# Optimization experiments

Hardware: AMD Instinct MI355X
Metric: run time of the kernel (lower is better)

## Reference

```python
import jax, jax.numpy as jnp
import numpy as np


def _gcn_conv(x, W, b, src, dst, dinv):
    # h = x @ W, then symmetric-normalized aggregation with self-loops (PyG GCNConv)
    n = x.shape[0]
    h = x @ W  # [N, H]
    norm_e = dinv[src] * dinv[dst]  # [E]
    msgs = h[src] * norm_e[:, None]  # [E, H] gathered+scaled messages
    agg = jax.ops.segment_sum(msgs, dst, num_segments=n)
    # self-loop contribution: norm = dinv[i]^2
    agg = agg + h * (dinv * dinv)[:, None]
    return agg + b


def setup_inputs() -> dict:
    key = jax.random.key(0)
    k1, k2, k3, k4, k5 = jax.random.split(key, 5)
    N, E, C_in, H = 50000, 800000, 256, 128
    x = jax.random.normal(k1, (N, C_in), dtype=jnp.float32)
    edge_index = jax.random.randint(k2, (2, E), 0, N, dtype=jnp.int32)
    s = 1.0 / np.sqrt(C_in)
    W1 = jax.random.uniform(k3, (C_in, H), jnp.float32, -s, s)
    b1 = jnp.zeros((H,), jnp.float32)
    s2 = 1.0 / np.sqrt(H)
    W_mu = jax.random.uniform(k4, (H, H), jnp.float32, -s2, s2)
    b_mu = jnp.zeros((H,), jnp.float32)
    W_ls = jax.random.uniform(k5, (H, H), jnp.float32, -s2, s2)
    b_ls = jnp.zeros((H,), jnp.float32)
    return {"x": x, "edge_index": edge_index, "W1": W1, "b1": b1,
            "W_mu": W_mu, "b_mu": b_mu, "W_ls": W_ls, "b_ls": b_ls}


def reference(x, edge_index, W1, b1, W_mu, b_mu, W_ls, b_ls):
    n = x.shape[0]
    src, dst = edge_index[0], edge_index[1]
    # degree with self-loops (count incoming edges at target + 1)
    deg = jax.ops.segment_sum(jnp.ones_like(dst, dtype=x.dtype), dst, num_segments=n) + 1.0
    dinv = jax.lax.rsqrt(deg)
    h = jax.nn.relu(_gcn_conv(x, W1, b1, src, dst, dinv))
    mu = _gcn_conv(h, W_mu, b_mu, src, dst, dinv)
    logstd = _gcn_conv(h, W_ls, b_ls, src, dst, dinv)
    return mu, logstd
```

## Files before the change

### kernel.cpp

```cpp
#include <hip/hip_runtime.h>
#include <hip/hip_bf16.h>
#include <cstdint>

#define HFEAT 128
#define CIN   256

typedef unsigned int  uint;
typedef unsigned short ushort;
typedef short bf16x8 __attribute__((ext_vector_type(8)));
typedef float f32x4  __attribute__((ext_vector_type(4)));

__device__ inline float bflo(uint u){ return __uint_as_float(u << 16); }
__device__ inline float bfhi(uint u){ return __uint_as_float(u & 0xffff0000u); }
__device__ inline uint  f2bf(float f){
  union { __hip_bfloat16 b; ushort u; } cvt;
  cvt.b = __float2bfloat16(f);
  return (uint)cvt.u;
}


__global__ void k_count(const int* __restrict__ dst, int E, int* __restrict__ counts){
  int e = blockIdx.x*blockDim.x + threadIdx.x;
  if (e < E) atomicAdd(&counts[dst[e]], 1);
}

__global__ void k_scan1(const int* __restrict__ counts, int n,
                        int* __restrict__ excl, int* __restrict__ bsum,
                        float* __restrict__ dinv){
  __shared__ int sm[1024];
  int t = threadIdx.x;
  int i = blockIdx.x*1024 + t;
  int v = (i < n) ? counts[i] : 0;
  if (i < n) dinv[i] = rsqrtf((float)v + 1.0f);
  sm[t] = v;
  __syncthreads();
  for (int off = 1; off < 1024; off <<= 1){
    int add = (t >= off) ? sm[t-off] : 0;
    __syncthreads();
    sm[t] += add;
    __syncthreads();
  }
  if (i < n) excl[i] = sm[t] - v;
  if (t == 1023) bsum[blockIdx.x] = sm[t];
}

__global__ void k_scan2(int* __restrict__ bsum, int nb){
  if (threadIdx.x == 0 && blockIdx.x == 0){
    int run = 0;
    for (int b = 0; b < nb; b++){ int v = bsum[b]; bsum[b] = run; run += v; }
  }
}

__global__ void k_scan3(const int* __restrict__ bsum, int n, int E,
                        int* __restrict__ rowoff, int* __restrict__ cursor){
  int i = blockIdx.x*blockDim.x + threadIdx.x;
  if (i < n){
    int v = rowoff[i] + bsum[blockIdx.x];
    rowoff[i] = v;
    cursor[i] = v;
  }
  if (i == 0) rowoff[n] = E;
}

__global__ void k_fill(const int* __restrict__ src, const int* __restrict__ dst, int E,
                       int* __restrict__ cursor, int* __restrict__ csr4){
  int e = blockIdx.x*blockDim.x + threadIdx.x;
  if (e < E){
    int pos = atomicAdd(&cursor[dst[e]], 1);
    csr4[pos] = src[e];
  }
}


__global__ void k_cvt_all(const float* __restrict__ W1,  const float* __restrict__ Wmu,
                          const float* __restrict__ Wls, ushort* __restrict__ W1t,
                          ushort* __restrict__ Wmut, ushort* __restrict__ Wlst){
  int b = blockIdx.x, t = threadIdx.x;
  if (b < 128){
    W1t[b * CIN + t] = (ushort)f2bf(W1[(size_t)t * HFEAT + b]);
  } else if (b < 256){
    int nn = b - 128;
    if (t < HFEAT) Wmut[nn * HFEAT + t] = (ushort)f2bf(Wmu[(size_t)t * HFEAT + nn]);
  } else {
    int nn = b - 256;
    if (t < HFEAT) Wlst[nn * HFEAT + t] = (ushort)f2bf(Wls[(size_t)t * HFEAT + nn]);
  }
}


template<int K, bool IN_BF16, bool BIAS, bool OUT_BF16, bool SCALE_DINV>
__global__ void __launch_bounds__(256) k_gemm_mfma(const void* __restrict__ Ain,
                                                   const ushort* __restrict__ Wta,
                                                   const ushort* __restrict__ Wtb,
                                                   const float* __restrict__ ba,
                                                   const float* __restrict__ bb,
                                                   const float* __restrict__ dinv,
                                                   void* __restrict__ outa,
                                                   void* __restrict__ outb,
                                                   int n){
  __shared__ ushort Abuf[64][72];
  __shared__ ushort Bbuf[128][72];

  const ushort* Wt   = (blockIdx.y == 0) ? Wta : Wtb;
  const float*  bias = (blockIdx.y == 0) ? ba  : bb;
  void*         outv = (blockIdx.y == 0) ? outa : outb;

  const int tid  = threadIdx.x;
  const int w    = tid >> 6;
  const int l    = tid & 63;
  const int l15  = l & 15;
  const int lhi  = l >> 4;
  const int row0 = blockIdx.x * 64;

  const int ar = tid >> 2;
  const int aq = tid & 3;
  int arow = row0 + ar; if (arow >= n) arow = n - 1;

  f32x4 acc[8];
  #pragma unroll
  for (int t = 0; t < 8; t++) acc[t] = (f32x4){0.f, 0.f, 0.f, 0.f};

  const int NT = K / 64;
  #pragma unroll
  for (int kt = 0; kt < NT; ++kt){
    if (IN_BF16){
      const ushort* ap = (const ushort*)Ain + (size_t)arow * K + aq * 16 + kt * 64;
      uint4 v0 = *(const uint4*)(ap);
      uint4 v1 = *(const uint4*)(ap + 8);
      *(uint4*)&Abuf[ar][aq * 16]     = v0;
      *(uint4*)&Abuf[ar][aq * 16 + 8] = v1;
    } else {
      const float* p = (const float*)Ain + (size_t)arow * K + aq * 16 + kt * 64;
      float4 v0 = *(const float4*)(p);
      float4 v1 = *(const float4*)(p + 4);
      float4 v2 = *(const float4*)(p + 8);
      float4 v3 = *(const float4*)(p + 12);
      uint4 pa, pb;
      pa.x = f2bf(v0.x) | (f2bf(v0.y) << 16);
      pa.y = f2bf(v0.z) | (f2bf(v0.w) << 16);
      pa.z = f2bf(v1.x) | (f2bf(v1.y) << 16);
      pa.w = f2bf(v1.z) | (f2bf(v1.w) << 16);
      pb.x = f2bf(v2.x) | (f2bf(v2.y) << 16);
      pb.y = f2bf(v2.z) | (f2bf(v2.w) << 16);
      pb.z = f2bf(v3.x) | (f2bf(v3.y) << 16);
      pb.w = f2bf(v3.z) | (f2bf(v3.w) << 16);
      *(uint4*)&Abuf[ar][aq * 16]     = pa;
      *(uint4*)&Abuf[ar][aq * 16 + 8] = pb;
    }
    #pragma unroll
    for (int j = 0; j < 4; ++j){
      int flat = tid + 256 * j;
      int bn = flat >> 3;
      int bk = (flat & 7) * 8;
      uint4 v = *(const uint4*)(Wt + (size_t)bn * K + kt * 64 + bk);
      *(uint4*)&Bbuf[bn][bk] = v;
    }
    __syncthreads();

    #pragma unroll
    for (int ks = 0; ks < 2; ++ks){
      const int ko = ks * 32 + lhi * 8;
      bf16x8 af = *(bf16x8*)&Abuf[16 * w + l15][ko];
      #pragma unroll
      for (int nt = 0; nt < 8; ++nt){
        bf16x8 bf = *(bf16x8*)&Bbuf[nt * 16 + l15][ko];
        acc[nt] = __builtin_amdgcn_mfma_f32_16x16x32_bf16(af, bf, acc[nt], 0, 0, 0);
      }
    }
    __syncthreads();
  }

  float bv[8];
  #pragma unroll
  for (int nt = 0; nt < 8; ++nt) bv[nt] = BIAS ? bias[nt * 16 + l15] : 0.f;

  #pragma unroll
  for (int j = 0; j < 4; ++j){
    int r = row0 + 16 * w + lhi * 4 + j;
    if (r < n){
      float sc = SCALE_DINV ? dinv[r] : 1.f;
      if (OUT_BF16){
        ushort* orow = (ushort*)outv + (size_t)r * HFEAT + l15;
        #pragma unroll
        for (int nt = 0; nt < 8; ++nt)
          orow[nt * 16] = (ushort)f2bf((acc[nt][j] + bv[nt]) * sc);
      } else {
        float* orow = (float*)outv + (size_t)r * HFEAT + l15;
        #pragma unroll
        for (int nt = 0; nt < 8; ++nt)
          orow[nt * 16] = acc[nt][j] + bv[nt];
      }
    }
  }
}


template<int RELU>
__global__ void __launch_bounds__(256) k_agg(const ushort* __restrict__ in,
                                             const float* __restrict__ bias,
                                             const int* __restrict__ rowoff,
                                             const int* __restrict__ csr4,
                                             const float* __restrict__ dinv,
                                             ushort* __restrict__ out, int n){
  int gid  = blockIdx.x*blockDim.x + threadIdx.x;
  int node = gid >> 6;
  int lane = gid & 63;
  if (node >= n) return;
  const int w  = lane >> 4;
  const int q  = lane & 15;
  const int f0 = q * 8;

  float acc[8] = {0,0,0,0,0,0,0,0};

  const int e0 = rowoff[node], e1 = rowoff[node+1];
  #pragma unroll 2
  for (int e = e0 + w; e < e1; e += 4){
    int s = csr4[e];
    uint4 v = *(const uint4*)(in + ((size_t)s << 7) + f0);
    acc[0] += bflo(v.x); acc[1] += bfhi(v.x);
    acc[2] += bflo(v.y); acc[3] += bfhi(v.y);
    acc[4] += bflo(v.z); acc[5] += bfhi(v.z);
    acc[6] += bflo(v.w); acc[7] += bfhi(v.w);
  }
  if (w == 0){
    uint4 v = *(const uint4*)(in + ((size_t)node << 7) + f0);
    acc[0] += bflo(v.x); acc[1] += bfhi(v.x);
    acc[2] += bflo(v.y); acc[3] += bfhi(v.y);
    acc[4] += bflo(v.z); acc[5] += bfhi(v.z);
    acc[6] += bflo(v.w); acc[7] += bfhi(v.w);
  }
  #pragma unroll
  for (int j = 0; j < 8; j++){
    acc[j] += __shfl_xor(acc[j], 16);
    acc[j] += __shfl_xor(acc[j], 32);
  }

  if (w == 0){
    float di = dinv[node];
    uint4 p;
    if (RELU){
      float4 b0 = *(const float4*)&bias[f0];
      float4 b1 = *(const float4*)&bias[f0 + 4];
      float r0 = fmaxf(fmaf(acc[0], di, b0.x), 0.f) * di;
      float r1 = fmaxf(fmaf(acc[1], di, b0.y), 0.f) * di;
      float r2 = fmaxf(fmaf(acc[2], di, b0.z), 0.f) * di;
      float r3 = fmaxf(fmaf(acc[3], di, b0.w), 0.f) * di;
      float r4 = fmaxf(fmaf(acc[4], di, b1.x), 0.f) * di;
      float r5 = fmaxf(fmaf(acc[5], di, b1.y), 0.f) * di;
      float r6 = fmaxf(fmaf(acc[6], di, b1.z), 0.f) * di;
      float r7 = fmaxf(fmaf(acc[7], di, b1.w), 0.f) * di;
      p.x = f2bf(r0) | (f2bf(r1) << 16);
      p.y = f2bf(r2) | (f2bf(r3) << 16);
      p.z = f2bf(r4) | (f2bf(r5) << 16);
      p.w = f2bf(r6) | (f2bf(r7) << 16);
    } else {
      p.x = f2bf(acc[0] * di) | (f2bf(acc[1] * di) << 16);
      p.y = f2bf(acc[2] * di) | (f2bf(acc[3] * di) << 16);
      p.z = f2bf(acc[4] * di) | (f2bf(acc[5] * di) << 16);
      p.w = f2bf(acc[6] * di) | (f2bf(acc[7] * di) << 16);
    }
    *(uint4*)(out + ((size_t)node << 7) + f0) = p;
  }
}


extern "C" void kernel_launch(void* const* d_in, const int* in_sizes, int n_in,
                              void* d_out, int out_size, void* d_ws, size_t ws_size,
                              hipStream_t stream){
  const float* x   = (const float*)d_in[0];
  const int*   ei  = (const int*)  d_in[1];
  const float* W1  = (const float*)d_in[2];
  const float* b1  = (const float*)d_in[3];
  const float* Wmu = (const float*)d_in[4];
  const float* bmu = (const float*)d_in[5];
  const float* Wls = (const float*)d_in[6];
  const float* bls = (const float*)d_in[7];
  int N = in_sizes[0] / CIN;
  int E = in_sizes[1] / 2;
  const int* src = ei;
  const int* dst = ei + E;
  float* out = (float*)d_out;

  char* w = (char*)d_ws;
  auto alloc = [&](size_t bytes)->char*{
    char* p = w; w += (bytes + 255) & ~(size_t)255; return p;
  };
  ushort* t1    = (ushort*)alloc((size_t)N*HFEAT*2);
  ushort* t2    = (ushort*)alloc((size_t)N*HFEAT*2);
  ushort* gb    = (ushort*)alloc((size_t)N*HFEAT*2);
  ushort* W1bt  = (ushort*)alloc((size_t)HFEAT*CIN*2);
  ushort* Wmut  = (ushort*)alloc((size_t)HFEAT*HFEAT*2);
  ushort* Wlst  = (ushort*)alloc((size_t)HFEAT*HFEAT*2);
  int*   counts = (int*)   alloc((size_t)N*4);
  float* dinv   = (float*) alloc((size_t)N*4);
  int*   rowoff = (int*)   alloc(((size_t)N+1)*4);
  int*   cursor = (int*)   alloc((size_t)N*4);
  int*   bsum   = (int*)   alloc(256*4);
  int*   csr4   = (int*)   alloc((size_t)E*4);

  int nbE  = (E + 255) / 256;
  int nbS  = (N + 1023) / 1024;
  int nbG  = (N + 63) / 64;

  hipMemsetAsync(counts, 0, (size_t)N*4, stream);
  k_count   <<<nbE, 256, 0, stream>>>(dst, E, counts);
  k_scan1   <<<nbS, 1024, 0, stream>>>(counts, N, rowoff, bsum, dinv);
  k_scan2   <<<1, 64, 0, stream>>>(bsum, nbS);
  k_scan3   <<<nbS, 1024, 0, stream>>>(bsum, N, E, rowoff, cursor);
  k_fill    <<<nbE, 256, 0, stream>>>(src, dst, E, cursor, csr4);
  k_cvt_all <<<384, 256, 0, stream>>>(W1, Wmu, Wls, W1bt, Wmut, Wlst);

  k_gemm_mfma<CIN, false, false, true, true><<<dim3(nbG, 1), 256, 0, stream>>>(
      x, W1bt, W1bt, nullptr, nullptr, dinv, t1, t1, N);
  int aggBlocks = (int)(((size_t)N*64 + 255) / 256);
  k_agg<1><<<aggBlocks, 256, 0, stream>>>(t1, b1, rowoff, csr4, dinv, t2, N);
  k_agg<0><<<aggBlocks, 256, 0, stream>>>(t2, nullptr, rowoff, csr4, dinv, gb, N);
  k_gemm_mfma<HFEAT, true, true, false, false><<<dim3(nbG, 2), 256, 0, stream>>>(
      gb, Wmut, Wlst, bmu, bls, nullptr, out, out + (size_t)N*HFEAT, N);
}
```

Measured before the change: 295.3 us.

## Fuse degree count with first GEMM and build CSR from atomic ranks

Edge degree counting now runs in the same launch as the first MFMA GEMM, and each atomic increment records the edge's rank. Because of that, the per-row dinv scaling moves out of the GEMM epilogue and into the aggregation as a per-edge dinv[src] weight. The CSR fill writes each edge to rowoff plus its rank with no second atomic pass. Source indices are stored as 16-bit values to halve index traffic, which only works while N stays below 65536. The serial block-sum scan becomes a shared-memory parallel scan, and the aggregation gains one extra dinv gather per edge.

```diff
diff --git a/kernel.cpp b/kernel.cpp
--- a/kernel.cpp
+++ b/kernel.cpp
@@ -18,11 +18,6 @@
   return (uint)cvt.u;
 }
 
-
-__global__ void k_count(const int* __restrict__ dst, int E, int* __restrict__ counts){
-  int e = blockIdx.x*blockDim.x + threadIdx.x;
-  if (e < E) atomicAdd(&counts[dst[e]], 1);
-}
 
 __global__ void k_scan1(const int* __restrict__ counts, int n,
                         int* __restrict__ excl, int* __restrict__ bsum,
@@ -45,30 +40,32 @@
 }
 
 __global__ void k_scan2(int* __restrict__ bsum, int nb){
-  if (threadIdx.x == 0 && blockIdx.x == 0){
-    int run = 0;
-    for (int b = 0; b < nb; b++){ int v = bsum[b]; bsum[b] = run; run += v; }
-  }
+  __shared__ int sm[1024];
+  int t = threadIdx.x;
+  int v = (t < nb) ? bsum[t] : 0;
+  sm[t] = v;
+  __syncthreads();
+  for (int off = 1; off < 1024; off <<= 1){
+    int add = (t >= off) ? sm[t-off] : 0;
+    __syncthreads();
+    sm[t] += add;
+    __syncthreads();
+  }
+  if (t < nb) bsum[t] = sm[t] - v;
 }
 
 __global__ void k_scan3(const int* __restrict__ bsum, int n, int E,
-                        int* __restrict__ rowoff, int* __restrict__ cursor){
+                        int* __restrict__ rowoff){
   int i = blockIdx.x*blockDim.x + threadIdx.x;
-  if (i < n){
-    int v = rowoff[i] + bsum[blockIdx.x];
-    rowoff[i] = v;
-    cursor[i] = v;
-  }
+  if (i < n) rowoff[i] += bsum[blockIdx.x];
   if (i == 0) rowoff[n] = E;
 }
 
-__global__ void k_fill(const int* __restrict__ src, const int* __restrict__ dst, int E,
-                       int* __restrict__ cursor, int* __restrict__ csr4){
+__global__ void k_fill(const int* __restrict__ src, const int* __restrict__ dst,
+                       const int* __restrict__ rank, int E,
+                       const int* __restrict__ rowoff, ushort* __restrict__ csr2){
   int e = blockIdx.x*blockDim.x + threadIdx.x;
-  if (e < E){
-    int pos = atomicAdd(&cursor[dst[e]], 1);
-    csr4[pos] = src[e];
-  }
+  if (e < E) csr2[rowoff[dst[e]] + rank[e]] = (ushort)src[e];
 }
 
 
@@ -88,29 +85,20 @@
 }
 
 
-template<int K, bool IN_BF16, bool BIAS, bool OUT_BF16, bool SCALE_DINV>
-__global__ void __launch_bounds__(256) k_gemm_mfma(const void* __restrict__ Ain,
-                                                   const ushort* __restrict__ Wta,
-                                                   const ushort* __restrict__ Wtb,
-                                                   const float* __restrict__ ba,
-                                                   const float* __restrict__ bb,
-                                                   const float* __restrict__ dinv,
-                                                   void* __restrict__ outa,
-                                                   void* __restrict__ outb,
-                                                   int n){
-  __shared__ ushort Abuf[64][72];
-  __shared__ ushort Bbuf[128][72];
-
-  const ushort* Wt   = (blockIdx.y == 0) ? Wta : Wtb;
-  const float*  bias = (blockIdx.y == 0) ? ba  : bb;
-  void*         outv = (blockIdx.y == 0) ? outa : outb;
-
+template<int K, bool IN_BF16, bool BIAS, bool OUT_BF16>
+__device__ __forceinline__ void gemm_body(int bid,
+                                          const void* __restrict__ Ain,
+                                          const ushort* __restrict__ Wt,
+                                          const float* __restrict__ bias,
+                                          void* __restrict__ outv,
+                                          int n,
+                                          ushort (*Abuf)[72], ushort (*Bbuf)[72]){
   const int tid  = threadIdx.x;
   const int w    = tid >> 6;
   const int l    = tid & 63;
   const int l15  = l & 15;
   const int lhi  = l >> 4;
-  const int row0 = blockIdx.x * 64;
+  const int row0 = bid * 64;
 
   const int ar = tid >> 2;
   const int aq = tid & 3;
@@ -178,12 +166,11 @@
   for (int j = 0; j < 4; ++j){
     int r = row0 + 16 * w + lhi * 4 + j;
     if (r < n){
-      float sc = SCALE_DINV ? dinv[r] : 1.f;
       if (OUT_BF16){
         ushort* orow = (ushort*)outv + (size_t)r * HFEAT + l15;
         #pragma unroll
         for (int nt = 0; nt < 8; ++nt)
-          orow[nt * 16] = (ushort)f2bf((acc[nt][j] + bv[nt]) * sc);
+          orow[nt * 16] = (ushort)f2bf(acc[nt][j] + bv[nt]);
       } else {
         float* orow = (float*)outv + (size_t)r * HFEAT + l15;
         #pragma unroll
@@ -195,11 +182,47 @@
 }
 
 
+__global__ void __launch_bounds__(256) k_count_gemm1(const int* __restrict__ dst, int E,
+                                                     int* __restrict__ counts,
+                                                     int* __restrict__ rank,
+                                                     int nbE,
+                                                     const float* __restrict__ x,
+                                                     const ushort* __restrict__ W1t,
+                                                     ushort* __restrict__ t1, int n){
+  __shared__ ushort Abuf[64][72];
+  __shared__ ushort Bbuf[128][72];
+  int b = blockIdx.x;
+  if (b < nbE){
+    int e = b * 256 + threadIdx.x;
+    if (e < E) rank[e] = atomicAdd(&counts[dst[e]], 1);
+    return;
+  }
+  gemm_body<CIN, false, false, true>(b - nbE, x, W1t, nullptr, t1, n, Abuf, Bbuf);
+}
+
+template<int K, bool IN_BF16, bool BIAS, bool OUT_BF16>
+__global__ void __launch_bounds__(256) k_gemm_mfma(const void* __restrict__ Ain,
+                                                   const ushort* __restrict__ Wta,
+                                                   const ushort* __restrict__ Wtb,
+                                                   const float* __restrict__ ba,
+                                                   const float* __restrict__ bb,
+                                                   void* __restrict__ outa,
+                                                   void* __restrict__ outb,
+                                                   int n){
+  __shared__ ushort Abuf[64][72];
+  __shared__ ushort Bbuf[128][72];
+  const ushort* Wt   = (blockIdx.y == 0) ? Wta : Wtb;
+  const float*  bias = (blockIdx.y == 0) ? ba  : bb;
+  void*         outv = (blockIdx.y == 0) ? outa : outb;
+  gemm_body<K, IN_BF16, BIAS, OUT_BF16>(blockIdx.x, Ain, Wt, bias, outv, n, Abuf, Bbuf);
+}
+
+
 template<int RELU>
 __global__ void __launch_bounds__(256) k_agg(const ushort* __restrict__ in,
                                              const float* __restrict__ bias,
                                              const int* __restrict__ rowoff,
-                                             const int* __restrict__ csr4,
+                                             const ushort* __restrict__ csr2,
                                              const float* __restrict__ dinv,
                                              ushort* __restrict__ out, int n){
   int gid  = blockIdx.x*blockDim.x + threadIdx.x;
@@ -215,19 +238,29 @@
   const int e0 = rowoff[node], e1 = rowoff[node+1];
   #pragma unroll 2
   for (int e = e0 + w; e < e1; e += 4){
-    int s = csr4[e];
+    int s = (int)csr2[e];
+    float wv = dinv[s];
     uint4 v = *(const uint4*)(in + ((size_t)s << 7) + f0);
-    acc[0] += bflo(v.x); acc[1] += bfhi(v.x);
-    acc[2] += bflo(v.y); acc[3] += bfhi(v.y);
-    acc[4] += bflo(v.z); acc[5] += bfhi(v.z);
-    acc[6] += bflo(v.w); acc[7] += bfhi(v.w);
+    acc[0] = fmaf(bflo(v.x), wv, acc[0]);
+    acc[1] = fmaf(bfhi(v.x), wv, acc[1]);
+    acc[2] = fmaf(bflo(v.y), wv, acc[2]);
+    acc[3] = fmaf(bfhi(v.y), wv, acc[3]);
+    acc[4] = fmaf(bflo(v.z), wv, acc[4]);
+    acc[5] = fmaf(bfhi(v.z), wv, acc[5]);
+    acc[6] = fmaf(bflo(v.w), wv, acc[6]);
+    acc[7] = fmaf(bfhi(v.w), wv, acc[7]);
   }
   if (w == 0){
+    float di = dinv[node];
     uint4 v = *(const uint4*)(in + ((size_t)node << 7) + f0);
-    acc[0] += bflo(v.x); acc[1] += bfhi(v.x);
-    acc[2] += bflo(v.y); acc[3] += bfhi(v.y);
-    acc[4] += bflo(v.z); acc[5] += bfhi(v.z);
-    acc[6] += bflo(v.w); acc[7] += bfhi(v.w);
+    acc[0] = fmaf(bflo(v.x), di, acc[0]);
+    acc[1] = fmaf(bfhi(v.x), di, acc[1]);
+    acc[2] = fmaf(bflo(v.y), di, acc[2]);
+    acc[3] = fmaf(bfhi(v.y), di, acc[3]);
+    acc[4] = fmaf(bflo(v.z), di, acc[4]);
+    acc[5] = fmaf(bfhi(v.z), di, acc[5]);
+    acc[6] = fmaf(bflo(v.w), di, acc[6]);
+    acc[7] = fmaf(bfhi(v.w), di, acc[7]);
   }
   #pragma unroll
   for (int j = 0; j < 8; j++){
@@ -241,14 +274,14 @@
     if (RELU){
       float4 b0 = *(const float4*)&bias[f0];
       float4 b1 = *(const float4*)&bias[f0 + 4];
-      float r0 = fmaxf(fmaf(acc[0], di, b0.x), 0.f) * di;
-      float r1 = fmaxf(fmaf(acc[1], di, b0.y), 0.f) * di;
-      float r2 = fmaxf(fmaf(acc[2], di, b0.z), 0.f) * di;
-      float r3 = fmaxf(fmaf(acc[3], di, b0.w), 0.f) * di;
-      float r4 = fmaxf(fmaf(acc[4], di, b1.x), 0.f) * di;
-      float r5 = fmaxf(fmaf(acc[5], di, b1.y), 0.f) * di;
-      float r6 = fmaxf(fmaf(acc[6], di, b1.z), 0.f) * di;
-      float r7 = fmaxf(fmaf(acc[7], di, b1.w), 0.f) * di;
+      float r0 = fmaxf(fmaf(acc[0], di, b0.x), 0.f);
+      float r1 = fmaxf(fmaf(acc[1], di, b0.y), 0.f);
+      float r2 = fmaxf(fmaf(acc[2], di, b0.z), 0.f);
+      float r3 = fmaxf(fmaf(acc[3], di, b0.w), 0.f);
+      float r4 = fmaxf(fmaf(acc[4], di, b1.x), 0.f);
+      float r5 = fmaxf(fmaf(acc[5], di, b1.y), 0.f);
+      float r6 = fmaxf(fmaf(acc[6], di, b1.z), 0.f);
+      float r7 = fmaxf(fmaf(acc[7], di, b1.w), 0.f);
       p.x = f2bf(r0) | (f2bf(r1) << 16);
       p.y = f2bf(r2) | (f2bf(r3) << 16);
       p.z = f2bf(r4) | (f2bf(r5) << 16);
@@ -294,27 +327,26 @@
   int*   counts = (int*)   alloc((size_t)N*4);
   float* dinv   = (float*) alloc((size_t)N*4);
   int*   rowoff = (int*)   alloc(((size_t)N+1)*4);
-  int*   cursor = (int*)   alloc((size_t)N*4);
-  int*   bsum   = (int*)   alloc(256*4);
-  int*   csr4   = (int*)   alloc((size_t)E*4);
+  int*   rank   = (int*)   alloc((size_t)E*4);
+  int*   bsum   = (int*)   alloc(1024*4);
+  ushort* csr2  = (ushort*)alloc((size_t)E*2);
 
   int nbE  = (E + 255) / 256;
   int nbS  = (N + 1023) / 1024;
   int nbG  = (N + 63) / 64;
 
   hipMemsetAsync(counts, 0, (size_t)N*4, stream);
-  k_count   <<<nbE, 256, 0, stream>>>(dst, E, counts);
+  k_cvt_all <<<384, 256, 0, stream>>>(W1, Wmu, Wls, W1bt, Wmut, Wlst);
+  k_count_gemm1<<<nbE + nbG, 256, 0, stream>>>(dst, E, counts, rank, nbE,
+                                               x, W1bt, t1, N);
   k_scan1   <<<nbS, 1024, 0, stream>>>(counts, N, rowoff, bsum, dinv);
-  k_scan2   <<<1, 64, 0, stream>>>(bsum, nbS);
-  k_scan3   <<<nbS, 1024, 0, stream>>>(bsum, N, E, rowoff, cursor);
-  k_fill    <<<nbE, 256, 0, stream>>>(src, dst, E, cursor, csr4);
-  k_cvt_all <<<384, 256, 0, stream>>>(W1, Wmu, Wls, W1bt, Wmut, Wlst);
-
-  k_gemm_mfma<CIN, false, false, true, true><<<dim3(nbG, 1), 256, 0, stream>>>(
-      x, W1bt, W1bt, nullptr, nullptr, dinv, t1, t1, N);
+  k_scan2   <<<1, 1024, 0, stream>>>(bsum, nbS);
+  k_scan3   <<<nbS, 1024, 0, stream>>>(bsum, N, E, rowoff);
+  k_fill    <<<nbE, 256, 0, stream>>>(src, dst, rank, E, rowoff, csr2);
+
   int aggBlocks = (int)(((size_t)N*64 + 255) / 256);
-  k_agg<1><<<aggBlocks, 256, 0, stream>>>(t1, b1, rowoff, csr4, dinv, t2, N);
-  k_agg<0><<<aggBlocks, 256, 0, stream>>>(t2, nullptr, rowoff, csr4, dinv, gb, N);
-  k_gemm_mfma<HFEAT, true, true, false, false><<<dim3(nbG, 2), 256, 0, stream>>>(
-      gb, Wmut, Wlst, bmu, bls, nullptr, out, out + (size_t)N*HFEAT, N);
-}
+  k_agg<1><<<aggBlocks, 256, 0, stream>>>(t1, b1, rowoff, csr2, dinv, t2, N);
+  k_agg<0><<<aggBlocks, 256, 0, stream>>>(t2, nullptr, rowoff, csr2, dinv, gb, N);
+  k_gemm_mfma<HFEAT, true, true, false><<<dim3(nbG, 2), 256, 0, stream>>>(
+      gb, Wmut, Wlst, bmu, bls, out, out + (size_t)N*HFEAT, N);
+}
```

Result: faster. 253.1 us (-14.3%).
